# Kernel tuning notes

Measured on AMD Instinct MI355X. Metric: run time of the kernel, lower is better.

Reference implementation:

```python
import jax, jax.numpy as jnp
import numpy as np


def setup_inputs() -> dict:
    key = jax.random.key(0)
    ks = jax.random.split(key, 10)
    B, L, H, E, D = 2, 2048, 16, 64, 64
    d_model = 512
    inp = {
        "queries": jax.random.normal(ks[0], (B, L, H, E), jnp.float32),
        "keys": jax.random.normal(ks[1], (B, L, H, E), jnp.float32),
        "values": jax.random.normal(ks[2], (B, L, H, D), jnp.float32),
        "raw_series": jax.random.normal(ks[3], (B, L, d_model), jnp.float32),
        # learned fusion MLP: Linear(d_model, d_model//2) -> ReLU -> Linear(d_model//2, 1)
        "w1": jax.random.normal(ks[4], (d_model, d_model // 2), jnp.float32) / np.sqrt(d_model),
        "b1": jnp.zeros((d_model // 2,), jnp.float32),
        "w2": jax.random.normal(ks[5], (d_model // 2, 1), jnp.float32) / np.sqrt(d_model // 2),
        "b2": jnp.zeros((1,), jnp.float32),
        # per-head trend scaling, init ones
        "alpha_trend": jnp.ones((H,), jnp.float32),
    }
    return inp


MOMENTUM_ALPHA = 1.0
MOMENTUM_K = 1


def reference(queries, keys, values, raw_series, w1, b1, w2, b2, alpha_trend):
    B, L, H, E = queries.shape
    scale = 1.0 / jnp.sqrt(jnp.asarray(E, queries.dtype))

    # ---- soft momentum bias ----
    # learned fusion: MLP over features -> scalar per position, [B, L]
    h = jax.nn.relu(raw_series @ w1 + b1)
    fused = (h @ w2 + b2)[..., 0]                       # [B, L]
    k = max(1, min(MOMENTUM_K, L - 1))
    momentum = fused[:, k:] - fused[:, :-k]              # [B, L-k]
    momentum = jnp.pad(momentum, ((0, 0), (k, 0)))       # left-pad zeros -> [B, L]
    diff = jnp.abs(momentum[:, :, None] - momentum[:, None, :])  # [B, L, L]
    soft_bias = -MOMENTUM_ALPHA * diff                   # [B, L, L]

    # ---- attention ----
    scores = jnp.einsum('blhe,bshe->bhls', queries, keys)  # [B, H, L, L]
    scores = scores + soft_bias[:, None, :, :] * alpha_trend[None, :, None, None]
    causal = jnp.triu(jnp.ones((L, L), bool), k=1)       # True above diagonal
    scores = jnp.where(causal[None, None], -jnp.inf, scores)
    A = jax.nn.softmax(scale * scores, axis=-1)          # [B, H, L, L]
    V = jnp.einsum('bhls,bshd->blhd', A, values)         # [B, L, H, D]
    return V
```

## Files before the change

### kernel.cpp

```cpp
#include <hip/hip_runtime.h>
#include <math.h>

#define B_ 2
#define L_ 2048
#define H_ 16
#define E_ 64
#define D_ 64
#define DM_ 512
#define DH_ 256

typedef __bf16 bf16_t;
typedef bf16_t bf16x8_t __attribute__((ext_vector_type(8)));
typedef float f32x4_t __attribute__((ext_vector_type(4)));

__device__ __forceinline__ unsigned bpack(float hi, float lo) {
    unsigned uh = __float_as_uint(hi) + 0x8000u;
    unsigned ul = __float_as_uint(lo) + 0x8000u;
    return __builtin_amdgcn_perm(uh, ul, 0x07060302u);
}

__device__ __forceinline__ bf16_t to_bf16(float f) {
    union { float f; unsigned u; } x; x.f = f;
    unsigned r = (x.u + 0x7fffu + ((x.u >> 16) & 1u)) >> 16;
    union { unsigned short s; bf16_t b; } y; y.s = (unsigned short)r;
    return y.b;
}

__global__ __launch_bounds__(256) void transpose_w1_kernel(
        const float* __restrict__ w1, bf16_t* __restrict__ w1t) {
    const int n = blockIdx.x;
    const int t = threadIdx.x;
    #pragma unroll
    for (int u = 0; u < 2; ++u) {
        int k = t + u * 256;
        float v = w1[(size_t)k * DH_ + n];
        w1t[(size_t)n * DM_ + k] = to_bf16(v);
    }
}

__global__ __launch_bounds__(256) void mlp_kernel(
        const float* __restrict__ raw, const bf16_t* __restrict__ w1t,
        const float* __restrict__ b1, const float* __restrict__ w2,
        const float* __restrict__ b2, float* __restrict__ fused) {
    __shared__ bf16_t Rs[16][520];
    __shared__ float part[4][16];
    const int t = threadIdx.x;
    const int m0 = blockIdx.x * 16;
    #pragma unroll
    for (int u = 0; u < 8; ++u) {
        int idx = t + u * 256;
        int row = idx >> 7;
        int k = (idx & 127) << 2;
        f32x4_t v = *(const f32x4_t*)&raw[(size_t)(m0 + row) * DM_ + k];
        uint2 p;
        p.x = bpack(v[1], v[0]);
        p.y = bpack(v[3], v[2]);
        *(uint2*)&Rs[row][k] = p;
    }
    __syncthreads();
    const int wave = t >> 6;
    const int lane = t & 63;
    const int lrow = lane & 15;
    const int lgrp = lane >> 4;
    const int n0w = wave * 64;

    f32x4_t acc[4];
    #pragma unroll
    for (int nt = 0; nt < 4; ++nt) acc[nt] = (f32x4_t){0.f, 0.f, 0.f, 0.f};

    const bf16_t* wbase = w1t + (size_t)(n0w + lrow) * DM_ + lgrp * 8;
    #pragma unroll
    for (int s = 0; s < 16; ++s) {
        bf16x8_t a = *(const bf16x8_t*)&Rs[lrow][s * 32 + lgrp * 8];
        #pragma unroll
        for (int nt = 0; nt < 4; ++nt) {
            bf16x8_t b = *(const bf16x8_t*)(wbase + nt * 16 * DM_ + s * 32);
            acc[nt] = __builtin_amdgcn_mfma_f32_16x16x32_bf16(a, b, acc[nt], 0, 0, 0);
        }
    }
    float rowpart[4] = {0.f, 0.f, 0.f, 0.f};
    #pragma unroll
    for (int nt = 0; nt < 4; ++nt) {
        int n = n0w + nt * 16 + lrow;
        float b1v = b1[n];
        float w2v = w2[n];
        #pragma unroll
        for (int r = 0; r < 4; ++r) {
            float h = acc[nt][r] + b1v;
            h = h > 0.f ? h : 0.f;
            rowpart[r] += h * w2v;
        }
    }
    #pragma unroll
    for (int r = 0; r < 4; ++r) {
        float v = rowpart[r];
        v += __shfl_xor(v, 1);
        v += __shfl_xor(v, 2);
        v += __shfl_xor(v, 4);
        v += __shfl_xor(v, 8);
        if (lrow == 0) part[wave][lgrp * 4 + r] = v;
    }
    __syncthreads();
    if (t < 16)
        fused[m0 + t] = part[0][t] + part[1][t] + part[2][t] + part[3][t] + b2[0];
}

__global__ __launch_bounds__(256) void momentum_kernel(
        const float* __restrict__ fused, float* __restrict__ mom) {
    int i = blockIdx.x * 256 + threadIdx.x;
    if (i < B_ * L_) {
        int l = i & (L_ - 1);
        mom[i] = (l == 0) ? 0.f : fused[i] - fused[i - 1];
    }
}

struct TileRegs { f32x4_t k[4]; float v[16]; float m; };

__global__ __launch_bounds__(256) void attn_kernel(
        const float* __restrict__ Q, const float* __restrict__ K,
        const float* __restrict__ V, const float* __restrict__ mom,
        const float* __restrict__ alpha_trend, float* __restrict__ out) {
    __shared__ __align__(16) bf16_t Ks[2][64][72];
    __shared__ __align__(16) bf16_t Vt[2][64][72];
    __shared__ __align__(16) float moms[2][64];

    const int bid  = blockIdx.x;
    const int bh   = bid & 31;
    const int qt   = 31 - (bid >> 5);
    const int h    = bh & 15;
    const int b    = bh >> 4;
    const int q0   = qt << 6;
    const int tid  = threadIdx.x;
    const int wave = tid >> 6;
    const int lane = tid & 63;
    const int lrow = lane & 15;
    const int lgrp = lane >> 4;

    const float c1      = 0.18033688f;
    const float ascale2 = alpha_trend[h] * c1;
    const size_t bl     = (size_t)b * L_;
    const int qw0       = q0 + wave * 16;

    const float* Kb   = K + (bl * H_ + h) * E_;
    const float* Vb   = V + (bl * H_ + h) * D_;
    const float* momp = mom + bl;

    const int krow = tid >> 4;
    const int ke0  = (tid & 15) << 2;
    const int p0   = (krow & 3) | (((krow >> 3) & 1) << 2) | (((krow >> 2) & 1) << 4);
    const int vd   = tid & 63;
    const int vsb  = tid >> 6;

    bf16x8_t a_lo, a_hi;
    {
        const float* qp = Q + ((bl + qw0 + lrow) * H_ + h) * E_ + lgrp * 8;
        f32x4_t v0 = *(const f32x4_t*)(qp);
        f32x4_t v1 = *(const f32x4_t*)(qp + 4);
        f32x4_t v2 = *(const f32x4_t*)(qp + 32);
        f32x4_t v3 = *(const f32x4_t*)(qp + 36);
        #pragma unroll
        for (int k = 0; k < 4; ++k) {
            a_lo[k]     = to_bf16(v0[k] * c1);
            a_lo[4 + k] = to_bf16(v1[k] * c1);
            a_hi[k]     = to_bf16(v2[k] * c1);
            a_hi[4 + k] = to_bf16(v3[k] * c1);
        }
    }
    const float mq = momp[qw0 + lrow];

    f32x4_t Oacc[4];
    #pragma unroll
    for (int c = 0; c < 4; ++c) Oacc[c] = (f32x4_t){0.f, 0.f, 0.f, 0.f};
    float rowsum = 0.f;

    TileRegs tr;
    {
        #pragma unroll
        for (int u = 0; u < 4; ++u)
            tr.k[u] = *(const f32x4_t*)&Kb[(krow + u * 16) * (H_ * E_) + ke0];
        #pragma unroll
        for (int j = 0; j < 16; ++j)
            tr.v[j] = Vb[(vsb * 16 + j) * (H_ * D_) + vd];
        tr.m = (tid < 64) ? momp[tid] : 0.f;
    }

    char* const vtbase = (char*)Vt;
    const int vswz = ((vd >> 3) & 7) << 4;

    for (int st = 0; st <= qt; ++st) {
        const int buf = st & 1;
        bf16_t (*Ksb)[72] = Ks[buf];
        char* vtb = vtbase + buf * (64 * 144);

        #pragma unroll
        for (int u = 0; u < 4; ++u) {
            uint2 p;
            p.x = bpack(tr.k[u][1], tr.k[u][0]);
            p.y = bpack(tr.k[u][3], tr.k[u][2]);
            int pr = p0 + (u & 1) * 8 + (u >> 1) * 32;
            *(uint2*)&Ksb[pr][ke0] = p;
        }
        #pragma unroll
        for (int u = 0; u < 4; ++u) {
            uint2 p;
            p.x = bpack(tr.v[u * 4 + 1], tr.v[u * 4 + 0]);
            p.y = bpack(tr.v[u * 4 + 3], tr.v[u * 4 + 2]);
            int boff = (vsb * 32 + u * 8) ^ vswz;
            *(uint2*)(vtb + vd * 144 + boff) = p;
        }
        if (tid < 64) moms[buf][tid] = tr.m;
        __syncthreads();

        if (st < qt) {
            const int s0n = (st + 1) << 6;
            #pragma unroll
            for (int u = 0; u < 4; ++u)
                tr.k[u] = *(const f32x4_t*)&Kb[(s0n + krow + u * 16) * (H_ * E_) + ke0];
            #pragma unroll
            for (int j = 0; j < 16; ++j)
                tr.v[j] = Vb[(s0n + vsb * 16 + j) * (H_ * D_) + vd];
            tr.m = (tid < 64) ? momp[s0n + tid] : 0.f;
        }

        f32x4_t Sacc[4];
        #pragma unroll
        for (int c = 0; c < 4; ++c) Sacc[c] = (f32x4_t){0.f, 0.f, 0.f, 0.f};
        #pragma unroll
        for (int c = 0; c < 4; ++c) {
            bf16x8_t k_lo = *(const bf16x8_t*)&Ksb[c * 16 + lrow][lgrp * 8];
            bf16x8_t k_hi = *(const bf16x8_t*)&Ksb[c * 16 + lrow][32 + lgrp * 8];
            Sacc[c] = __builtin_amdgcn_mfma_f32_16x16x32_bf16(k_lo, a_lo, Sacc[c], 0, 0, 0);
            Sacc[c] = __builtin_amdgcn_mfma_f32_16x16x32_bf16(k_hi, a_hi, Sacc[c], 0, 0, 0);
        }

        float rowe[4][4];
        #pragma unroll
        for (int c = 0; c < 4; ++c) {
            const int sb = lgrp * 8 + ((c & 1) << 2) + ((c >> 1) << 5);
            f32x4_t ms4 = *(const f32x4_t*)&moms[buf][sb];
            #pragma unroll
            for (int r = 0; r < 4; ++r) {
                float arg = Sacc[c][r] - ascale2 * fabsf(mq - ms4[r]);
                rowe[c][r] = __builtin_amdgcn_exp2f(arg);
            }
        }
        if (st == qt) {
            const int qg = qw0 + lrow;
            const int s0 = st << 6;
            #pragma unroll
            for (int c = 0; c < 4; ++c) {
                const int sg0 = s0 + lgrp * 8 + ((c & 1) << 2) + ((c >> 1) << 5);
                #pragma unroll
                for (int r = 0; r < 4; ++r)
                    if (sg0 + r > qg) rowe[c][r] = 0.f;
            }
        }
        #pragma unroll
        for (int c = 0; c < 4; ++c)
            rowsum += (rowe[c][0] + rowe[c][1]) + (rowe[c][2] + rowe[c][3]);

        #pragma unroll
        for (int hh = 0; hh < 2; ++hh) {
            union { unsigned u[4]; bf16x8_t v; } pa;
            pa.u[0] = bpack(rowe[2 * hh][1],     rowe[2 * hh][0]);
            pa.u[1] = bpack(rowe[2 * hh][3],     rowe[2 * hh][2]);
            pa.u[2] = bpack(rowe[2 * hh + 1][1], rowe[2 * hh + 1][0]);
            pa.u[3] = bpack(rowe[2 * hh + 1][3], rowe[2 * hh + 1][2]);
            #pragma unroll
            for (int c2 = 0; c2 < 4; ++c2) {
                const int row = c2 * 16 + lrow;
                int boff = (hh * 64 + lgrp * 16) ^ (((row >> 3) & 7) << 4);
                bf16x8_t bv = *(const bf16x8_t*)(vtb + row * 144 + boff);
                Oacc[c2] = __builtin_amdgcn_mfma_f32_16x16x32_bf16(pa.v, bv, Oacc[c2], 0, 0, 0);
            }
        }
    }

    float rs = rowsum;
    rs += __shfl_xor(rs, 16);
    rs += __shfl_xor(rs, 32);
    #pragma unroll
    for (int r = 0; r < 4; ++r) {
        float inv = 1.f / __shfl(rs, lgrp * 4 + r);
        size_t orow = ((bl + qw0 + lgrp * 4 + r) * H_ + h) * D_;
        #pragma unroll
        for (int c = 0; c < 4; ++c)
            out[orow + c * 16 + lrow] = Oacc[c][r] * inv;
    }
}

extern "C" void kernel_launch(void* const* d_in, const int* in_sizes, int n_in,
                              void* d_out, int out_size, void* d_ws, size_t ws_size,
                              hipStream_t stream) {
    const float* Q     = (const float*)d_in[0];
    const float* K     = (const float*)d_in[1];
    const float* V     = (const float*)d_in[2];
    const float* raw   = (const float*)d_in[3];
    const float* w1    = (const float*)d_in[4];
    const float* b1    = (const float*)d_in[5];
    const float* w2    = (const float*)d_in[6];
    const float* b2    = (const float*)d_in[7];
    const float* alpha = (const float*)d_in[8];
    float* out = (float*)d_out;

    float* fused = (float*)d_ws;
    float* mom   = fused + B_ * L_;
    bf16_t* w1t  = (bf16_t*)(mom + B_ * L_);

    transpose_w1_kernel<<<DH_, 256, 0, stream>>>(w1, w1t);
    mlp_kernel<<<B_ * L_ / 16, 256, 0, stream>>>(raw, w1t, b1, w2, b2, fused);
    momentum_kernel<<<(B_ * L_ + 255) / 256, 256, 0, stream>>>(fused, mom);
    attn_kernel<<<B_ * H_ * (L_ / 64), 256, 0, stream>>>(Q, K, V, mom, alpha, out);
}
```

Baseline: 162.3 us.

## Pre-convert K/V to swizzled bf16 and stream tiles via global_load_lds

A new prep kernel converts K to bf16 in a permuted, XOR-swizzled tile layout and V to a transposed bf16 layout once, instead of every attention block reconverting fp32 K/V from global memory. The attention kernel then copies tiles straight into LDS with global_load_lds, which drops the register staging and packing work. The momentum kernel is folded into the attention kernel, the query-tile order is interleaved for load balance, and setprio is placed around the MFMA sections. In exchange it adds a pre-pass and extra workspace traffic.

```diff
diff --git a/kernel.cpp b/kernel.cpp
--- a/kernel.cpp
+++ b/kernel.cpp
@@ -26,15 +26,90 @@
     return y.b;
 }
 
-__global__ __launch_bounds__(256) void transpose_w1_kernel(
-        const float* __restrict__ w1, bf16_t* __restrict__ w1t) {
-    const int n = blockIdx.x;
+__device__ __forceinline__ void gload_lds16(const bf16_t* g, bf16_t* l) {
+    __builtin_amdgcn_global_load_lds(
+        (const __attribute__((address_space(1))) unsigned int*)g,
+        (__attribute__((address_space(3))) unsigned int*)l, 16, 0, 0);
+}
+
+__device__ __forceinline__ int permK(int sl) {
+    return (sl & 3) | (((sl >> 3) & 1) << 2) | (((sl >> 4) & 1) << 3)
+         | (((sl >> 2) & 1) << 4) | (((sl >> 5) & 1) << 5);
+}
+
+__global__ __launch_bounds__(256) void prep_kernel(
+        const float* __restrict__ w1, bf16_t* __restrict__ w1t,
+        const float* __restrict__ K, bf16_t* __restrict__ Kp,
+        const float* __restrict__ V, bf16_t* __restrict__ Vs) {
+    __shared__ bf16_t T[64][88];
+    const int bidx = blockIdx.x;
     const int t = threadIdx.x;
-    #pragma unroll
-    for (int u = 0; u < 2; ++u) {
-        int k = t + u * 256;
-        float v = w1[(size_t)k * DH_ + n];
-        w1t[(size_t)n * DM_ + k] = to_bf16(v);
+
+    if (bidx < 256) {
+        const int n = bidx;
+        #pragma unroll
+        for (int u = 0; u < 2; ++u) {
+            int k = t + u * 256;
+            w1t[(size_t)n * DM_ + k] = to_bf16(w1[(size_t)k * DH_ + n]);
+        }
+        return;
+    }
+
+    if (bidx < 1280) {
+        const int idx = bidx - 256;
+        const int bh = idx >> 5, tile = idx & 31;
+        const int b = bh >> 4, h = bh & 15;
+        const int sl = t >> 2, e0 = (t & 3) << 4;
+        const float* src = K + (((size_t)b * L_ + tile * 64 + sl) * H_ + h) * E_ + e0;
+        f32x4_t v0 = *(const f32x4_t*)(src);
+        f32x4_t v1 = *(const f32x4_t*)(src + 4);
+        f32x4_t v2 = *(const f32x4_t*)(src + 8);
+        f32x4_t v3 = *(const f32x4_t*)(src + 12);
+        uint4 lo, hi;
+        lo.x = bpack(v0[1], v0[0]); lo.y = bpack(v0[3], v0[2]);
+        lo.z = bpack(v1[1], v1[0]); lo.w = bpack(v1[3], v1[2]);
+        hi.x = bpack(v2[1], v2[0]); hi.y = bpack(v2[3], v2[2]);
+        hi.z = bpack(v3[1], v3[0]); hi.w = bpack(v3[3], v3[2]);
+        const int r = permK(sl);
+        const int bb = (r >> 3) & 7;
+        bf16_t* drow = Kp + ((size_t)(bh * 32 + tile) * 64 + r) * 64;
+        *(uint4*)(drow + ((((e0 >> 3)    ) ^ bb) << 3)) = lo;
+        *(uint4*)(drow + ((((e0 >> 3) + 1) ^ bb) << 3)) = hi;
+        return;
+    }
+
+    {
+        const int idx = bidx - 1280;
+        const int bh = idx >> 5, tile = idx & 31;
+        const int b = bh >> 4, h = bh & 15;
+        const int sl = t >> 2, d0 = (t & 3) << 4;
+        const float* src = V + (((size_t)b * L_ + tile * 64 + sl) * H_ + h) * D_ + d0;
+        f32x4_t v0 = *(const f32x4_t*)(src);
+        f32x4_t v1 = *(const f32x4_t*)(src + 4);
+        f32x4_t v2 = *(const f32x4_t*)(src + 8);
+        f32x4_t v3 = *(const f32x4_t*)(src + 12);
+        uint4 lo, hi;
+        lo.x = bpack(v0[1], v0[0]); lo.y = bpack(v0[3], v0[2]);
+        lo.z = bpack(v1[1], v1[0]); lo.w = bpack(v1[3], v1[2]);
+        hi.x = bpack(v2[1], v2[0]); hi.y = bpack(v2[3], v2[2]);
+        hi.z = bpack(v3[1], v3[0]); hi.w = bpack(v3[3], v3[2]);
+        *(uint4*)&T[sl][d0]     = lo;
+        *(uint4*)&T[sl][d0 + 8] = hi;
+        __syncthreads();
+        const int d = t & 63, bd = (d >> 3) & 7;
+        bf16_t* drow = Vs + ((size_t)bh * 64 + d) * 2048 + tile * 64;
+        #pragma unroll
+        for (int gg = 0; gg < 2; ++gg) {
+            int qb = (t >> 6) + gg * 4;
+            int slb = (qb ^ bd) << 3;
+            union { unsigned short u[8]; uint4 q; } acc;
+            #pragma unroll
+            for (int j = 0; j < 8; ++j) {
+                union { bf16_t b; unsigned short s; } x; x.b = T[slb + j][d];
+                acc.u[j] = x.s;
+            }
+            *(uint4*)(drow + qb * 8) = acc.q;
+        }
     }
 }
 
@@ -105,51 +180,33 @@
         fused[m0 + t] = part[0][t] + part[1][t] + part[2][t] + part[3][t] + b2[0];
 }
 
-__global__ __launch_bounds__(256) void momentum_kernel(
-        const float* __restrict__ fused, float* __restrict__ mom) {
-    int i = blockIdx.x * 256 + threadIdx.x;
-    if (i < B_ * L_) {
-        int l = i & (L_ - 1);
-        mom[i] = (l == 0) ? 0.f : fused[i] - fused[i - 1];
-    }
-}
-
-struct TileRegs { f32x4_t k[4]; float v[16]; float m; };
-
 __global__ __launch_bounds__(256) void attn_kernel(
-        const float* __restrict__ Q, const float* __restrict__ K,
-        const float* __restrict__ V, const float* __restrict__ mom,
+        const float* __restrict__ Q, const bf16_t* __restrict__ Kp,
+        const bf16_t* __restrict__ Vs, const float* __restrict__ fused,
         const float* __restrict__ alpha_trend, float* __restrict__ out) {
-    __shared__ __align__(16) bf16_t Ks[2][64][72];
-    __shared__ __align__(16) bf16_t Vt[2][64][72];
-    __shared__ __align__(16) float moms[2][64];
-
-    const int bid  = blockIdx.x;
-    const int bh   = bid & 31;
-    const int qt   = 31 - (bid >> 5);
-    const int h    = bh & 15;
-    const int b    = bh >> 4;
-    const int q0   = qt << 6;
-    const int tid  = threadIdx.x;
-    const int wave = tid >> 6;
-    const int lane = tid & 63;
-    const int lrow = lane & 15;
-    const int lgrp = lane >> 4;
-
-    const float c1      = 0.18033688f;
+    __shared__ __align__(16) bf16_t Ks[2][64][64];
+    __shared__ __align__(16) bf16_t Vt[2][64][64];
+    __shared__ float moms[2][64];
+
+    const int bid = blockIdx.x;
+    const int bh  = bid & 31;
+    const int grp = bid >> 5;
+    const int qt  = (grp & 1) ? (grp >> 1) : 31 - (grp >> 1);
+    const int h = bh & 15, b = bh >> 4;
+    const int q0 = qt << 6;
+    const int tid = threadIdx.x;
+    const int wave = tid >> 6, lane = tid & 63;
+    const int lrow = lane & 15, lgrp = lane >> 4;
+    const int t8 = lrow >> 3;
+
+    const float c1 = 0.18033688f;
     const float ascale2 = alpha_trend[h] * c1;
-    const size_t bl     = (size_t)b * L_;
-    const int qw0       = q0 + wave * 16;
-
-    const float* Kb   = K + (bl * H_ + h) * E_;
-    const float* Vb   = V + (bl * H_ + h) * D_;
-    const float* momp = mom + bl;
-
-    const int krow = tid >> 4;
-    const int ke0  = (tid & 15) << 2;
-    const int p0   = (krow & 3) | (((krow >> 3) & 1) << 2) | (((krow >> 2) & 1) << 4);
-    const int vd   = tid & 63;
-    const int vsb  = tid >> 6;
+    const size_t bl = (size_t)b * L_;
+    const int qw0 = q0 + wave * 16;
+
+    const bf16_t* Kb = Kp + (size_t)bh * 131072;
+    const bf16_t* Vb = Vs + (size_t)bh * 131072;
+    const float* fusedp = fused + bl;
 
     bf16x8_t a_lo, a_hi;
     {
@@ -166,72 +223,57 @@
             a_hi[4 + k] = to_bf16(v3[k] * c1);
         }
     }
-    const float mq = momp[qw0 + lrow];
+    const int qg = qw0 + lrow;
+    const float mq = (qg == 0) ? 0.f : fusedp[qg] - fusedp[qg - 1];
+
+    const bf16_t* ksrc = Kb + wave * 512 + lane * 8;
+    const bf16_t* vsrc = Vb + (size_t)(wave * 8 + (lane >> 3)) * 2048 + (lane & 7) * 8;
 
     f32x4_t Oacc[4];
     #pragma unroll
     for (int c = 0; c < 4; ++c) Oacc[c] = (f32x4_t){0.f, 0.f, 0.f, 0.f};
     float rowsum = 0.f;
 
-    TileRegs tr;
-    {
-        #pragma unroll
-        for (int u = 0; u < 4; ++u)
-            tr.k[u] = *(const f32x4_t*)&Kb[(krow + u * 16) * (H_ * E_) + ke0];
-        #pragma unroll
-        for (int j = 0; j < 16; ++j)
-            tr.v[j] = Vb[(vsb * 16 + j) * (H_ * D_) + vd];
-        tr.m = (tid < 64) ? momp[tid] : 0.f;
-    }
-
-    char* const vtbase = (char*)Vt;
-    const int vswz = ((vd >> 3) & 7) << 4;
-
+    auto stage = [&](int t) {
+        const int nb = t & 1;
+        const bf16_t* kp0 = ksrc + (size_t)t * 4096;
+        gload_lds16(kp0,        &Ks[nb][wave * 8][0]);
+        gload_lds16(kp0 + 2048, &Ks[nb][wave * 8 + 32][0]);
+        const bf16_t* vp0 = vsrc + t * 64;
+        gload_lds16(vp0,               &Vt[nb][wave * 8][0]);
+        gload_lds16(vp0 + 32 * 2048,   &Vt[nb][wave * 8 + 32][0]);
+        if (tid < 64) {
+            int s = t * 64 + tid;
+            float f = fusedp[s];
+            float fm = __shfl_up(f, 1);
+            if (tid == 0) fm = (s == 0) ? f : fusedp[s - 1];
+            moms[nb][tid] = f - fm;
+        }
+    };
+
+    stage(0);
     for (int st = 0; st <= qt; ++st) {
         const int buf = st & 1;
-        bf16_t (*Ksb)[72] = Ks[buf];
-        char* vtb = vtbase + buf * (64 * 144);
-
-        #pragma unroll
-        for (int u = 0; u < 4; ++u) {
-            uint2 p;
-            p.x = bpack(tr.k[u][1], tr.k[u][0]);
-            p.y = bpack(tr.k[u][3], tr.k[u][2]);
-            int pr = p0 + (u & 1) * 8 + (u >> 1) * 32;
-            *(uint2*)&Ksb[pr][ke0] = p;
-        }
-        #pragma unroll
-        for (int u = 0; u < 4; ++u) {
-            uint2 p;
-            p.x = bpack(tr.v[u * 4 + 1], tr.v[u * 4 + 0]);
-            p.y = bpack(tr.v[u * 4 + 3], tr.v[u * 4 + 2]);
-            int boff = (vsb * 32 + u * 8) ^ vswz;
-            *(uint2*)(vtb + vd * 144 + boff) = p;
-        }
-        if (tid < 64) moms[buf][tid] = tr.m;
         __syncthreads();
-
-        if (st < qt) {
-            const int s0n = (st + 1) << 6;
-            #pragma unroll
-            for (int u = 0; u < 4; ++u)
-                tr.k[u] = *(const f32x4_t*)&Kb[(s0n + krow + u * 16) * (H_ * E_) + ke0];
-            #pragma unroll
-            for (int j = 0; j < 16; ++j)
-                tr.v[j] = Vb[(s0n + vsb * 16 + j) * (H_ * D_) + vd];
-            tr.m = (tid < 64) ? momp[s0n + tid] : 0.f;
-        }
+        if (st < qt) stage(st + 1);
+
+        const char* ksb = (const char*)&Ks[buf][0][0];
+        const char* vtb = (const char*)&Vt[buf][0][0];
 
         f32x4_t Sacc[4];
         #pragma unroll
         for (int c = 0; c < 4; ++c) Sacc[c] = (f32x4_t){0.f, 0.f, 0.f, 0.f};
+        __builtin_amdgcn_s_setprio(1);
         #pragma unroll
         for (int c = 0; c < 4; ++c) {
-            bf16x8_t k_lo = *(const bf16x8_t*)&Ksb[c * 16 + lrow][lgrp * 8];
-            bf16x8_t k_hi = *(const bf16x8_t*)&Ksb[c * 16 + lrow][32 + lgrp * 8];
+            const char* kr = ksb + (c * 16 + lrow) * 128;
+            const int bb = (c * 2 + t8) & 7;
+            bf16x8_t k_lo = *(const bf16x8_t*)(kr + ((lgrp ^ bb) << 4));
+            bf16x8_t k_hi = *(const bf16x8_t*)(kr + (((4 + lgrp) ^ bb) << 4));
             Sacc[c] = __builtin_amdgcn_mfma_f32_16x16x32_bf16(k_lo, a_lo, Sacc[c], 0, 0, 0);
             Sacc[c] = __builtin_amdgcn_mfma_f32_16x16x32_bf16(k_hi, a_hi, Sacc[c], 0, 0, 0);
         }
+        __builtin_amdgcn_s_setprio(0);
 
         float rowe[4][4];
         #pragma unroll
@@ -245,7 +287,6 @@
             }
         }
         if (st == qt) {
-            const int qg = qw0 + lrow;
             const int s0 = st << 6;
             #pragma unroll
             for (int c = 0; c < 4; ++c) {
@@ -266,13 +307,16 @@
             pa.u[1] = bpack(rowe[2 * hh][3],     rowe[2 * hh][2]);
             pa.u[2] = bpack(rowe[2 * hh + 1][1], rowe[2 * hh + 1][0]);
             pa.u[3] = bpack(rowe[2 * hh + 1][3], rowe[2 * hh + 1][2]);
+            __builtin_amdgcn_s_setprio(1);
             #pragma unroll
             for (int c2 = 0; c2 < 4; ++c2) {
                 const int row = c2 * 16 + lrow;
-                int boff = (hh * 64 + lgrp * 16) ^ (((row >> 3) & 7) << 4);
-                bf16x8_t bv = *(const bf16x8_t*)(vtb + row * 144 + boff);
+                const int bb2 = (c2 * 2 + t8) & 7;
+                bf16x8_t bv = *(const bf16x8_t*)(vtb + row * 128 +
+                                                 (((hh * 4 + lgrp) ^ bb2) << 4));
                 Oacc[c2] = __builtin_amdgcn_mfma_f32_16x16x32_bf16(pa.v, bv, Oacc[c2], 0, 0, 0);
             }
+            __builtin_amdgcn_s_setprio(0);
         }
     }
 
@@ -304,11 +348,11 @@
     float* out = (float*)d_out;
 
     float* fused = (float*)d_ws;
-    float* mom   = fused + B_ * L_;
-    bf16_t* w1t  = (bf16_t*)(mom + B_ * L_);
-
-    transpose_w1_kernel<<<DH_, 256, 0, stream>>>(w1, w1t);
+    bf16_t* w1t  = (bf16_t*)(fused + B_ * L_);
+    bf16_t* Kp   = w1t + 256 * 512;
+    bf16_t* Vs   = Kp + (size_t)B_ * H_ * L_ * E_;
+
+    prep_kernel<<<2304, 256, 0, stream>>>(w1, w1t, K, Kp, V, Vs);
     mlp_kernel<<<B_ * L_ / 16, 256, 0, stream>>>(raw, w1t, b1, w2, b2, fused);
-    momentum_kernel<<<(B_ * L_ + 255) / 256, 256, 0, stream>>>(fused, mom);
-    attn_kernel<<<B_ * H_ * (L_ / 64), 256, 0, stream>>>(Q, K, V, mom, alpha, out);
-}
+    attn_kernel<<<B_ * H_ * (L_ / 64), 256, 0, stream>>>(Q, Kp, Vs, fused, alpha, out);
+}
```

After: 184.3 us. 13.5% more time.

## Fuse MLP, momentum and attention into one persistent kernel with grid barrier

Applied to the files above, without the earlier changes.

Replaces four launches (w1 transpose, MLP, momentum, attention) with a single 512-block kernel. Each block first computes a slice of the fusion MLP, converting w1 on the fly instead of pre-transposing it, and writes four partial sums. A global atomic barrier then separates the MLP phase from the attention phase. In the attention phase each block handles two query tiles (grp and 31-grp) to balance causal work, rebuilds momentum values from the partial sums, and raises wave priority around the MFMA sections. The aim is to remove launch gaps and the intermediate kernels. The risks are a deadlock if all 512 blocks are not co-resident, strided uncoalesced w1 reads, and an extra memset launch.

```diff
diff --git a/kernel.cpp b/kernel.cpp
--- a/kernel.cpp
+++ b/kernel.cpp
@@ -8,6 +8,7 @@
 #define D_ 64
 #define DM_ 512
 #define DH_ 256
+#define GRID_ 512
 
 typedef __bf16 bf16_t;
 typedef bf16_t bf16x8_t __attribute__((ext_vector_type(8)));
@@ -26,266 +27,260 @@
     return y.b;
 }
 
-__global__ __launch_bounds__(256) void transpose_w1_kernel(
-        const float* __restrict__ w1, bf16_t* __restrict__ w1t) {
-    const int n = blockIdx.x;
-    const int t = threadIdx.x;
-    #pragma unroll
-    for (int u = 0; u < 2; ++u) {
-        int k = t + u * 256;
-        float v = w1[(size_t)k * DH_ + n];
-        w1t[(size_t)n * DM_ + k] = to_bf16(v);
+struct TileRegs { f32x4_t k[4]; float v[16]; float m; };
+
+__global__ __launch_bounds__(256, 4) void fused_kernel(
+        const float* __restrict__ Q, const float* __restrict__ K,
+        const float* __restrict__ V, const float* __restrict__ raw,
+        const float* __restrict__ w1, const float* __restrict__ b1,
+        const float* __restrict__ w2, const float* __restrict__ alpha_trend,
+        float* __restrict__ fused4, int* __restrict__ bar,
+        float* __restrict__ out) {
+    __shared__ union {
+        struct { bf16_t Ks[2][64][72]; bf16_t Vt[2][64][72]; float moms[2][64]; } a;
+        struct { bf16_t Rs[16][520]; float part[4][16]; } m;
+    } S;
+
+    const int tid = threadIdx.x;
+    const int bid = blockIdx.x;
+    const int wave = tid >> 6, lane = tid & 63;
+    const int lrow = lane & 15, lgrp = lane >> 4;
+
+    {
+        const int m0 = (bid >> 1) * 16;
+        const int nq0 = (bid & 1) << 1;
+        #pragma unroll
+        for (int u = 0; u < 8; ++u) {
+            int idx = tid + u * 256;
+            int row = idx >> 7;
+            int k = (idx & 127) << 2;
+            f32x4_t v = *(const f32x4_t*)&raw[(size_t)(m0 + row) * DM_ + k];
+            uint2 p;
+            p.x = bpack(v[1], v[0]);
+            p.y = bpack(v[3], v[2]);
+            *(uint2*)&S.m.Rs[row][k] = p;
+        }
+        __syncthreads();
+        #pragma unroll
+        for (int qq = 0; qq < 2; ++qq) {
+            const int nq = nq0 + qq;
+            const int n = nq * 64 + wave * 16 + lrow;
+            f32x4_t acc = (f32x4_t){0.f, 0.f, 0.f, 0.f};
+            const float* wcol = w1 + n;
+            #pragma unroll
+            for (int s = 0; s < 16; ++s) {
+                bf16x8_t a = *(const bf16x8_t*)&S.m.Rs[lrow][s * 32 + lgrp * 8];
+                const float* wp = wcol + (size_t)(s * 32 + lgrp * 8) * DH_;
+                bf16x8_t bfr;
+                #pragma unroll
+                for (int j = 0; j < 8; ++j) bfr[j] = to_bf16(wp[(size_t)j * DH_]);
+                acc = __builtin_amdgcn_mfma_f32_16x16x32_bf16(a, bfr, acc, 0, 0, 0);
+            }
+            const float b1v = b1[n];
+            const float w2v = w2[n];
+            float rowpart[4];
+            #pragma unroll
+            for (int r = 0; r < 4; ++r) {
+                float hh = acc[r] + b1v;
+                hh = hh > 0.f ? hh : 0.f;
+                rowpart[r] = hh * w2v;
+            }
+            #pragma unroll
+            for (int r = 0; r < 4; ++r) {
+                float v = rowpart[r];
+                v += __shfl_xor(v, 1);
+                v += __shfl_xor(v, 2);
+                v += __shfl_xor(v, 4);
+                v += __shfl_xor(v, 8);
+                if (lrow == 0) S.m.part[wave][lgrp * 4 + r] = v;
+            }
+            __syncthreads();
+            if (tid < 16)
+                fused4[nq * (B_ * L_) + m0 + tid] =
+                    S.m.part[0][tid] + S.m.part[1][tid] + S.m.part[2][tid] + S.m.part[3][tid];
+            __syncthreads();
+        }
     }
-}
-
-__global__ __launch_bounds__(256) void mlp_kernel(
-        const float* __restrict__ raw, const bf16_t* __restrict__ w1t,
-        const float* __restrict__ b1, const float* __restrict__ w2,
-        const float* __restrict__ b2, float* __restrict__ fused) {
-    __shared__ bf16_t Rs[16][520];
-    __shared__ float part[4][16];
-    const int t = threadIdx.x;
-    const int m0 = blockIdx.x * 16;
-    #pragma unroll
-    for (int u = 0; u < 8; ++u) {
-        int idx = t + u * 256;
-        int row = idx >> 7;
-        int k = (idx & 127) << 2;
-        f32x4_t v = *(const f32x4_t*)&raw[(size_t)(m0 + row) * DM_ + k];
-        uint2 p;
-        p.x = bpack(v[1], v[0]);
-        p.y = bpack(v[3], v[2]);
-        *(uint2*)&Rs[row][k] = p;
+
+    __threadfence();
+    __syncthreads();
+    if (tid == 0) {
+        __hip_atomic_fetch_add(bar, 1, __ATOMIC_ACQ_REL, __HIP_MEMORY_SCOPE_AGENT);
+        while (__hip_atomic_load(bar, __ATOMIC_ACQUIRE, __HIP_MEMORY_SCOPE_AGENT) < GRID_)
+            __builtin_amdgcn_s_sleep(2);
     }
     __syncthreads();
-    const int wave = t >> 6;
-    const int lane = t & 63;
-    const int lrow = lane & 15;
-    const int lgrp = lane >> 4;
-    const int n0w = wave * 64;
-
-    f32x4_t acc[4];
-    #pragma unroll
-    for (int nt = 0; nt < 4; ++nt) acc[nt] = (f32x4_t){0.f, 0.f, 0.f, 0.f};
-
-    const bf16_t* wbase = w1t + (size_t)(n0w + lrow) * DM_ + lgrp * 8;
-    #pragma unroll
-    for (int s = 0; s < 16; ++s) {
-        bf16x8_t a = *(const bf16x8_t*)&Rs[lrow][s * 32 + lgrp * 8];
-        #pragma unroll
-        for (int nt = 0; nt < 4; ++nt) {
-            bf16x8_t b = *(const bf16x8_t*)(wbase + nt * 16 * DM_ + s * 32);
-            acc[nt] = __builtin_amdgcn_mfma_f32_16x16x32_bf16(a, b, acc[nt], 0, 0, 0);
-        }
-    }
-    float rowpart[4] = {0.f, 0.f, 0.f, 0.f};
-    #pragma unroll
-    for (int nt = 0; nt < 4; ++nt) {
-        int n = n0w + nt * 16 + lrow;
-        float b1v = b1[n];
-        float w2v = w2[n];
-        #pragma unroll
-        for (int r = 0; r < 4; ++r) {
-            float h = acc[nt][r] + b1v;
-            h = h > 0.f ? h : 0.f;
-            rowpart[r] += h * w2v;
-        }
-    }
-    #pragma unroll
-    for (int r = 0; r < 4; ++r) {
-        float v = rowpart[r];
-        v += __shfl_xor(v, 1);
-        v += __shfl_xor(v, 2);
-        v += __shfl_xor(v, 4);
-        v += __shfl_xor(v, 8);
-        if (lrow == 0) part[wave][lgrp * 4 + r] = v;
-    }
-    __syncthreads();
-    if (t < 16)
-        fused[m0 + t] = part[0][t] + part[1][t] + part[2][t] + part[3][t] + b2[0];
-}
-
-__global__ __launch_bounds__(256) void momentum_kernel(
-        const float* __restrict__ fused, float* __restrict__ mom) {
-    int i = blockIdx.x * 256 + threadIdx.x;
-    if (i < B_ * L_) {
-        int l = i & (L_ - 1);
-        mom[i] = (l == 0) ? 0.f : fused[i] - fused[i - 1];
-    }
-}
-
-struct TileRegs { f32x4_t k[4]; float v[16]; float m; };
-
-__global__ __launch_bounds__(256) void attn_kernel(
-        const float* __restrict__ Q, const float* __restrict__ K,
-        const float* __restrict__ V, const float* __restrict__ mom,
-        const float* __restrict__ alpha_trend, float* __restrict__ out) {
-    __shared__ __align__(16) bf16_t Ks[2][64][72];
-    __shared__ __align__(16) bf16_t Vt[2][64][72];
-    __shared__ __align__(16) float moms[2][64];
-
-    const int bid  = blockIdx.x;
-    const int bh   = bid & 31;
-    const int qt   = 31 - (bid >> 5);
-    const int h    = bh & 15;
-    const int b    = bh >> 4;
-    const int q0   = qt << 6;
-    const int tid  = threadIdx.x;
-    const int wave = tid >> 6;
-    const int lane = tid & 63;
-    const int lrow = lane & 15;
-    const int lgrp = lane >> 4;
-
-    const float c1      = 0.18033688f;
+    __threadfence();
+
+    const int bh = bid & 31;
+    const int grp = bid >> 5;
+    const int h = bh & 15, b = bh >> 4;
+
+    const float c1 = 0.18033688f;
     const float ascale2 = alpha_trend[h] * c1;
-    const size_t bl     = (size_t)b * L_;
-    const int qw0       = q0 + wave * 16;
-
-    const float* Kb   = K + (bl * H_ + h) * E_;
-    const float* Vb   = V + (bl * H_ + h) * D_;
-    const float* momp = mom + bl;
+    const size_t bl = (size_t)b * L_;
+
+    const float* Kb = K + (bl * H_ + h) * E_;
+    const float* Vb = V + (bl * H_ + h) * D_;
+    const float* f4 = fused4 + bl;
+
+    auto fsum = [&](int i) {
+        return f4[i] + f4[4096 + i] + f4[8192 + i] + f4[12288 + i];
+    };
+    auto mom_at = [&](int i) { return (i > 0) ? fsum(i) - fsum(i - 1) : 0.f; };
 
     const int krow = tid >> 4;
     const int ke0  = (tid & 15) << 2;
     const int p0   = (krow & 3) | (((krow >> 3) & 1) << 2) | (((krow >> 2) & 1) << 4);
     const int vd   = tid & 63;
     const int vsb  = tid >> 6;
-
-    bf16x8_t a_lo, a_hi;
-    {
-        const float* qp = Q + ((bl + qw0 + lrow) * H_ + h) * E_ + lgrp * 8;
-        f32x4_t v0 = *(const f32x4_t*)(qp);
-        f32x4_t v1 = *(const f32x4_t*)(qp + 4);
-        f32x4_t v2 = *(const f32x4_t*)(qp + 32);
-        f32x4_t v3 = *(const f32x4_t*)(qp + 36);
+    const int vswz = ((vd >> 3) & 7) << 4;
+    char* const vtbase = (char*)S.a.Vt;
+
+    #pragma unroll 1
+    for (int half = 0; half < 2; ++half) {
+        const int qt = half ? (31 - grp) : grp;
+        const int q0 = qt << 6;
+        const int qw0 = q0 + wave * 16;
+        const int qg = qw0 + lrow;
+
+        bf16x8_t a_lo, a_hi;
+        {
+            const float* qp = Q + ((bl + qw0 + lrow) * H_ + h) * E_ + lgrp * 8;
+            f32x4_t v0 = *(const f32x4_t*)(qp);
+            f32x4_t v1 = *(const f32x4_t*)(qp + 4);
+            f32x4_t v2 = *(const f32x4_t*)(qp + 32);
+            f32x4_t v3 = *(const f32x4_t*)(qp + 36);
+            #pragma unroll
+            for (int k = 0; k < 4; ++k) {
+                a_lo[k]     = to_bf16(v0[k] * c1);
+                a_lo[4 + k] = to_bf16(v1[k] * c1);
+                a_hi[k]     = to_bf16(v2[k] * c1);
+                a_hi[4 + k] = to_bf16(v3[k] * c1);
+            }
+        }
+        const float mq = mom_at(qg);
+
+        f32x4_t Oacc[4];
         #pragma unroll
-        for (int k = 0; k < 4; ++k) {
-            a_lo[k]     = to_bf16(v0[k] * c1);
-            a_lo[4 + k] = to_bf16(v1[k] * c1);
-            a_hi[k]     = to_bf16(v2[k] * c1);
-            a_hi[4 + k] = to_bf16(v3[k] * c1);
-        }
-    }
-    const float mq = momp[qw0 + lrow];
-
-    f32x4_t Oacc[4];
-    #pragma unroll
-    for (int c = 0; c < 4; ++c) Oacc[c] = (f32x4_t){0.f, 0.f, 0.f, 0.f};
-    float rowsum = 0.f;
-
-    TileRegs tr;
-    {
+        for (int c = 0; c < 4; ++c) Oacc[c] = (f32x4_t){0.f, 0.f, 0.f, 0.f};
+        float rowsum = 0.f;
+
+        TileRegs tr;
+        {
+            #pragma unroll
+            for (int u = 0; u < 4; ++u)
+                tr.k[u] = *(const f32x4_t*)&Kb[(krow + u * 16) * (H_ * E_) + ke0];
+            #pragma unroll
+            for (int j = 0; j < 16; ++j)
+                tr.v[j] = Vb[(vsb * 16 + j) * (H_ * D_) + vd];
+            tr.m = (tid < 64) ? mom_at(tid) : 0.f;
+        }
+        __syncthreads();
+
+        for (int st = 0; st <= qt; ++st) {
+            const int buf = st & 1;
+            bf16_t (*Ksb)[72] = S.a.Ks[buf];
+            char* vtb = vtbase + buf * (64 * 144);
+
+            #pragma unroll
+            for (int u = 0; u < 4; ++u) {
+                uint2 p;
+                p.x = bpack(tr.k[u][1], tr.k[u][0]);
+                p.y = bpack(tr.k[u][3], tr.k[u][2]);
+                int pr = p0 + (u & 1) * 8 + (u >> 1) * 32;
+                *(uint2*)&Ksb[pr][ke0] = p;
+            }
+            #pragma unroll
+            for (int u = 0; u < 4; ++u) {
+                uint2 p;
+                p.x = bpack(tr.v[u * 4 + 1], tr.v[u * 4 + 0]);
+                p.y = bpack(tr.v[u * 4 + 3], tr.v[u * 4 + 2]);
+                int boff = (vsb * 32 + u * 8) ^ vswz;
+                *(uint2*)(vtb + vd * 144 + boff) = p;
+            }
+            if (tid < 64) S.a.moms[buf][tid] = tr.m;
+            __syncthreads();
+
+            if (st < qt) {
+                const int s0n = (st + 1) << 6;
+                #pragma unroll
+                for (int u = 0; u < 4; ++u)
+                    tr.k[u] = *(const f32x4_t*)&Kb[(s0n + krow + u * 16) * (H_ * E_) + ke0];
+                #pragma unroll
+                for (int j = 0; j < 16; ++j)
+                    tr.v[j] = Vb[(s0n + vsb * 16 + j) * (H_ * D_) + vd];
+                tr.m = (tid < 64) ? mom_at(s0n + tid) : 0.f;
+            }
+
+            f32x4_t Sacc[4];
+            #pragma unroll
+            for (int c = 0; c < 4; ++c) Sacc[c] = (f32x4_t){0.f, 0.f, 0.f, 0.f};
+            __builtin_amdgcn_s_setprio(1);
+            #pragma unroll
+            for (int c = 0; c < 4; ++c) {
+                bf16x8_t k_lo = *(const bf16x8_t*)&Ksb[c * 16 + lrow][lgrp * 8];
+                bf16x8_t k_hi = *(const bf16x8_t*)&Ksb[c * 16 + lrow][32 + lgrp * 8];
+                Sacc[c] = __builtin_amdgcn_mfma_f32_16x16x32_bf16(k_lo, a_lo, Sacc[c], 0, 0, 0);
+                Sacc[c] = __builtin_amdgcn_mfma_f32_16x16x32_bf16(k_hi, a_hi, Sacc[c], 0, 0, 0);
+            }
+            __builtin_amdgcn_s_setprio(0);
+
+            float rowe[4][4];
+            #pragma unroll
+            for (int c = 0; c < 4; ++c) {
+                const int sb = lgrp * 8 + ((c & 1) << 2) + ((c >> 1) << 5);
+                f32x4_t ms4 = *(const f32x4_t*)&S.a.moms[buf][sb];
+                #pragma unroll
+                for (int r = 0; r < 4; ++r) {
+                    float arg = Sacc[c][r] - ascale2 * fabsf(mq - ms4[r]);
+                    rowe[c][r] = __builtin_amdgcn_exp2f(arg);
+                }
+            }
+            if (st == qt) {
+                const int s0 = st << 6;
+                #pragma unroll
+                for (int c = 0; c < 4; ++c) {
+                    const int sg0 = s0 + lgrp * 8 + ((c & 1) << 2) + ((c >> 1) << 5);
+                    #pragma unroll
+                    for (int r = 0; r < 4; ++r)
+                        if (sg0 + r > qg) rowe[c][r] = 0.f;
+                }
+            }
+            #pragma unroll
+            for (int c = 0; c < 4; ++c)
+                rowsum += (rowe[c][0] + rowe[c][1]) + (rowe[c][2] + rowe[c][3]);
+
+            #pragma unroll
+            for (int hh = 0; hh < 2; ++hh) {
+                union { unsigned u[4]; bf16x8_t v; } pa;
+                pa.u[0] = bpack(rowe[2 * hh][1],     rowe[2 * hh][0]);
+                pa.u[1] = bpack(rowe[2 * hh][3],     rowe[2 * hh][2]);
+                pa.u[2] = bpack(rowe[2 * hh + 1][1], rowe[2 * hh + 1][0]);
+                pa.u[3] = bpack(rowe[2 * hh + 1][3], rowe[2 * hh + 1][2]);
+                __builtin_amdgcn_s_setprio(1);
+                #pragma unroll
+                for (int c2 = 0; c2 < 4; ++c2) {
+                    const int row = c2 * 16 + lrow;
+                    int boff = (hh * 64 + lgrp * 16) ^ (((row >> 3) & 7) << 4);
+                    bf16x8_t bv = *(const bf16x8_t*)(vtb + row * 144 + boff);
+                    Oacc[c2] = __builtin_amdgcn_mfma_f32_16x16x32_bf16(pa.v, bv, Oacc[c2], 0, 0, 0);
+                }
+                __builtin_amdgcn_s_setprio(0);
+            }
+        }
+
+        float rs = rowsum;
+        rs += __shfl_xor(rs, 16);
+        rs += __shfl_xor(rs, 32);
         #pragma unroll
-        for (int u = 0; u < 4; ++u)
-            tr.k[u] = *(const f32x4_t*)&Kb[(krow + u * 16) * (H_ * E_) + ke0];
-        #pragma unroll
-        for (int j = 0; j < 16; ++j)
-            tr.v[j] = Vb[(vsb * 16 + j) * (H_ * D_) + vd];
-        tr.m = (tid < 64) ? momp[tid] : 0.f;
-    }
-
-    char* const vtbase = (char*)Vt;
-    const int vswz = ((vd >> 3) & 7) << 4;
-
-    for (int st = 0; st <= qt; ++st) {
-        const int buf = st & 1;
-        bf16_t (*Ksb)[72] = Ks[buf];
-        char* vtb = vtbase + buf * (64 * 144);
-
-        #pragma unroll
-        for (int u = 0; u < 4; ++u) {
-            uint2 p;
-            p.x = bpack(tr.k[u][1], tr.k[u][0]);
-            p.y = bpack(tr.k[u][3], tr.k[u][2]);
-            int pr = p0 + (u & 1) * 8 + (u >> 1) * 32;
-            *(uint2*)&Ksb[pr][ke0] = p;
-        }
-        #pragma unroll
-        for (int u = 0; u < 4; ++u) {
-            uint2 p;
-            p.x = bpack(tr.v[u * 4 + 1], tr.v[u * 4 + 0]);
-            p.y = bpack(tr.v[u * 4 + 3], tr.v[u * 4 + 2]);
-            int boff = (vsb * 32 + u * 8) ^ vswz;
-            *(uint2*)(vtb + vd * 144 + boff) = p;
-        }
-        if (tid < 64) moms[buf][tid] = tr.m;
-        __syncthreads();
-
-        if (st < qt) {
-            const int s0n = (st + 1) << 6;
-            #pragma unroll
-            for (int u = 0; u < 4; ++u)
-                tr.k[u] = *(const f32x4_t*)&Kb[(s0n + krow + u * 16) * (H_ * E_) + ke0];
-            #pragma unroll
-            for (int j = 0; j < 16; ++j)
-                tr.v[j] = Vb[(s0n + vsb * 16 + j) * (H_ * D_) + vd];
-            tr.m = (tid < 64) ? momp[s0n + tid] : 0.f;
-        }
-
-        f32x4_t Sacc[4];
-        #pragma unroll
-        for (int c = 0; c < 4; ++c) Sacc[c] = (f32x4_t){0.f, 0.f, 0.f, 0.f};
-        #pragma unroll
-        for (int c = 0; c < 4; ++c) {
-            bf16x8_t k_lo = *(const bf16x8_t*)&Ksb[c * 16 + lrow][lgrp * 8];
-            bf16x8_t k_hi = *(const bf16x8_t*)&Ksb[c * 16 + lrow][32 + lgrp * 8];
-            Sacc[c] = __builtin_amdgcn_mfma_f32_16x16x32_bf16(k_lo, a_lo, Sacc[c], 0, 0, 0);
-            Sacc[c] = __builtin_amdgcn_mfma_f32_16x16x32_bf16(k_hi, a_hi, Sacc[c], 0, 0, 0);
-        }
-
-        float rowe[4][4];
-        #pragma unroll
-        for (int c = 0; c < 4; ++c) {
-            const int sb = lgrp * 8 + ((c & 1) << 2) + ((c >> 1) << 5);
-            f32x4_t ms4 = *(const f32x4_t*)&moms[buf][sb];
-            #pragma unroll
-            for (int r = 0; r < 4; ++r) {
-                float arg = Sacc[c][r] - ascale2 * fabsf(mq - ms4[r]);
-                rowe[c][r] = __builtin_amdgcn_exp2f(arg);
-            }
-        }
-        if (st == qt) {
-            const int qg = qw0 + lrow;
-            const int s0 = st << 6;
-            #pragma unroll
-            for (int c = 0; c < 4; ++c) {
-                const int sg0 = s0 + lgrp * 8 + ((c & 1) << 2) + ((c >> 1) << 5);
-                #pragma unroll
-                for (int r = 0; r < 4; ++r)
-                    if (sg0 + r > qg) rowe[c][r] = 0.f;
-            }
-        }
-        #pragma unroll
-        for (int c = 0; c < 4; ++c)
-            rowsum += (rowe[c][0] + rowe[c][1]) + (rowe[c][2] + rowe[c][3]);
-
-        #pragma unroll
-        for (int hh = 0; hh < 2; ++hh) {
-            union { unsigned u[4]; bf16x8_t v; } pa;
-            pa.u[0] = bpack(rowe[2 * hh][1],     rowe[2 * hh][0]);
-            pa.u[1] = bpack(rowe[2 * hh][3],     rowe[2 * hh][2]);
-            pa.u[2] = bpack(rowe[2 * hh + 1][1], rowe[2 * hh + 1][0]);
-            pa.u[3] = bpack(rowe[2 * hh + 1][3], rowe[2 * hh + 1][2]);
-            #pragma unroll
-            for (int c2 = 0; c2 < 4; ++c2) {
-                const int row = c2 * 16 + lrow;
-                int boff = (hh * 64 + lgrp * 16) ^ (((row >> 3) & 7) << 4);
-                bf16x8_t bv = *(const bf16x8_t*)(vtb + row * 144 + boff);
-                Oacc[c2] = __builtin_amdgcn_mfma_f32_16x16x32_bf16(pa.v, bv, Oacc[c2], 0, 0, 0);
-            }
-        }
-    }
-
-    float rs = rowsum;
-    rs += __shfl_xor(rs, 16);
-    rs += __shfl_xor(rs, 32);
-    #pragma unroll
-    for (int r = 0; r < 4; ++r) {
-        float inv = 1.f / __shfl(rs, lgrp * 4 + r);
-        size_t orow = ((bl + qw0 + lgrp * 4 + r) * H_ + h) * D_;
-        #pragma unroll
-        for (int c = 0; c < 4; ++c)
-            out[orow + c * 16 + lrow] = Oacc[c][r] * inv;
+        for (int r = 0; r < 4; ++r) {
+            float inv = 1.f / __shfl(rs, lgrp * 4 + r);
+            size_t orow = ((bl + qw0 + lgrp * 4 + r) * H_ + h) * D_;
+            #pragma unroll
+            for (int c = 0; c < 4; ++c)
+                out[orow + c * 16 + lrow] = Oacc[c][r] * inv;
+        }
     }
 }
 
@@ -299,16 +294,13 @@
     const float* w1    = (const float*)d_in[4];
     const float* b1    = (const float*)d_in[5];
     const float* w2    = (const float*)d_in[6];
-    const float* b2    = (const float*)d_in[7];
     const float* alpha = (const float*)d_in[8];
     float* out = (float*)d_out;
 
-    float* fused = (float*)d_ws;
-    float* mom   = fused + B_ * L_;
-    bf16_t* w1t  = (bf16_t*)(mom + B_ * L_);
-
-    transpose_w1_kernel<<<DH_, 256, 0, stream>>>(w1, w1t);
-    mlp_kernel<<<B_ * L_ / 16, 256, 0, stream>>>(raw, w1t, b1, w2, b2, fused);
-    momentum_kernel<<<(B_ * L_ + 255) / 256, 256, 0, stream>>>(fused, mom);
-    attn_kernel<<<B_ * H_ * (L_ / 64), 256, 0, stream>>>(Q, K, V, mom, alpha, out);
+    int*   bar    = (int*)d_ws;
+    float* fused4 = (float*)((char*)d_ws + 256);
+
+    hipMemsetAsync(bar, 0, 256, stream);
+    fused_kernel<<<GRID_, 256, 0, stream>>>(Q, K, V, raw, w1, b1, w2, alpha,
+                                            fused4, bar, out);
 }
```

Result: slower. 271.1 us (+67.1%).
